# Performance work log

Measured on AMD Instinct MI355X. Metric: run time of the kernel, lower is better.

The kernel has to match this reference:

```python
import jax, jax.numpy as jnp
import numpy as np

DMODEL = 2048
NUM_HEADS = 16
NUM_KV_HEADS = 4
HEAD_DIM = DMODEL // NUM_HEADS  # 128
THETA = 10000.0


def setup_inputs() -> dict:
    key = jax.random.key(0)
    k0, k1, k2, k3, k4 = jax.random.split(key, 5)
    B, S = 1, 4096
    x = jax.random.normal(k0, (B, S, DMODEL), dtype=jnp.float32)
    # Linear weights stored as [in, out] (equivalent to torch [out,in] with x @ W.T)
    sd = 0.02
    wq = jax.random.normal(k1, (DMODEL, NUM_HEADS * HEAD_DIM), dtype=jnp.float32) * sd
    wk = jax.random.normal(k2, (DMODEL, NUM_KV_HEADS * HEAD_DIM), dtype=jnp.float32) * sd
    wv = jax.random.normal(k3, (DMODEL, NUM_KV_HEADS * HEAD_DIM), dtype=jnp.float32) * sd
    wo = jax.random.normal(k4, (NUM_HEADS * HEAD_DIM, DMODEL), dtype=jnp.float32) * sd
    return {"x": x, "wq": wq, "wk": wk, "wv": wv, "wo": wo}


def _rope_cos_sin(seqlen, dtype):
    # RoPE.forward: inv_freq over half the head dim, emb = cat(freqs, freqs)
    inv_freq = 1.0 / (THETA ** (jnp.arange(0, HEAD_DIM, 2, dtype=jnp.float32) / HEAD_DIM))
    pos = jnp.arange(seqlen, dtype=jnp.float32)
    freqs = pos[:, None] * inv_freq[None, :]          # [S, HEAD_DIM/2]
    emb = jnp.concatenate([freqs, freqs], axis=-1)    # [S, HEAD_DIM]
    return emb.astype(dtype) * 0 + jnp.cos(emb).astype(dtype), jnp.sin(emb).astype(dtype)


def _rot(t):
    half = t.shape[-1] // 2
    return jnp.concatenate([-t[..., half:], t[..., :half]], axis=-1)


def reference(x, wq, wk, wv, wo):
    B, S, _ = x.shape
    q = (x @ wq).reshape(B, S, NUM_HEADS, HEAD_DIM).transpose(0, 2, 1, 3)      # [B,H,S,D]
    k = (x @ wk).reshape(B, S, NUM_KV_HEADS, HEAD_DIM).transpose(0, 2, 1, 3)   # [B,KV,S,D]
    v = (x @ wv).reshape(B, S, NUM_KV_HEADS, HEAD_DIM).transpose(0, 2, 1, 3)

    cos, sin = _rope_cos_sin(S, x.dtype)  # [S, D]
    cos = cos[None, None, :, :]
    sin = sin[None, None, :, :]
    q = q * cos + _rot(q) * sin
    k = k * cos + _rot(k) * sin

    rep = NUM_HEADS // NUM_KV_HEADS
    k = jnp.repeat(k, rep, axis=1)  # [B,H,S,D]
    v = jnp.repeat(v, rep, axis=1)

    scale = 1.0 / jnp.sqrt(jnp.asarray(HEAD_DIM, dtype=x.dtype))
    scores = jnp.einsum('bhqd,bhkd->bhqk', q, k) * scale
    causal = jnp.tril(jnp.ones((S, S), dtype=bool))
    scores = jnp.where(causal[None, None], scores, jnp.finfo(x.dtype).min)
    attn = jax.nn.softmax(scores, axis=-1)
    o = jnp.einsum('bhqk,bhkd->bhqd', attn, v)          # [B,H,S,D]
    o = o.transpose(0, 2, 1, 3).reshape(B, S, NUM_HEADS * HEAD_DIM)
    return o @ wo
```

## Files before the change

kernel.cpp:

```cpp
#include <hip/hip_runtime.h>
#include <math.h>

#define SEQ   4096
#define DM    2048
#define NH    16
#define NKV   4
#define HD    128
#define QKVN  3072
#define CEXP  0.12753643f

typedef _Float16 f16;
typedef _Float16 f16x8 __attribute__((ext_vector_type(8)));
typedef _Float16 f16x4v __attribute__((ext_vector_type(4)));
typedef float    f32x4 __attribute__((ext_vector_type(4)));

#define GLD16(g, l) __builtin_amdgcn_global_load_lds(                        \
    (const __attribute__((address_space(1))) unsigned int*)(g),              \
    (__attribute__((address_space(3))) unsigned int*)(l), 16, 0, 0)

__global__ __launch_bounds__(256) void cast_f32_f16_k(const float* __restrict__ in,
                                                      f16* __restrict__ out, int n4)
{
    int i = blockIdx.x * 256 + threadIdx.x;
    if (i >= n4) return;
    float4 v = ((const float4*)in)[i];
    f16x4v h = {(f16)v.x, (f16)v.y, (f16)v.z, (f16)v.w};
    ((f16x4v*)out)[i] = h;
}

__global__ __launch_bounds__(256) void transpose_cast_k(const float* __restrict__ in,
                                                        f16* __restrict__ out,
                                                        int R, int Cn, float scale)
{
    __shared__ float tile[32][33];
    int bx = blockIdx.x * 32, by = blockIdx.y * 32;
    int tx = threadIdx.x & 31, ty = threadIdx.x >> 5;
    #pragma unroll
    for (int i = 0; i < 32; i += 8)
        tile[ty + i][tx] = in[(size_t)(by + ty + i) * Cn + bx + tx];
    __syncthreads();
    #pragma unroll
    for (int i = 0; i < 32; i += 8)
        out[(size_t)(bx + ty + i) * R + by + tx] = (f16)(tile[tx][ty + i] * scale);
}

__global__ __launch_bounds__(256) void transpose_f16_k(const f16* __restrict__ in,
                                                       f16* __restrict__ out,
                                                       int R, int Cn, int ldin)
{
    __shared__ f16 tile[32][33];
    int bx = blockIdx.x * 32, by = blockIdx.y * 32;
    int tx = threadIdx.x & 31, ty = threadIdx.x >> 5;
    #pragma unroll
    for (int i = 0; i < 32; i += 8)
        tile[ty + i][tx] = in[(size_t)(by + ty + i) * ldin + bx + tx];
    __syncthreads();
    #pragma unroll
    for (int i = 0; i < 32; i += 8)
        out[(size_t)(bx + ty + i) * R + by + tx] = tile[tx][ty + i];
}

template <int BN, typename OutT>
__global__ __launch_bounds__(512, 2) void gemm8p(const f16* __restrict__ A,
                                                 const f16* __restrict__ Bt,
                                                 OutT* __restrict__ C,
                                                 int M, int N, int K)
{
    constexpr int LB  = (BN == 256) ? 2 : 1;
    constexpr int NF  = BN / 16;
    constexpr int NPP = NF / 4;
    (void)M;

    __shared__ __align__(16) f16 sm[32768 + 2 * BN * 64];
    f16* As = sm;
    f16* Bs = sm + 32768;

    const int t = threadIdx.x;
    const int w = t >> 6;
    const int lane = t & 63, ln = lane & 15, quad = lane >> 4;
    const size_t bm = (size_t)blockIdx.y * 256, bn = (size_t)blockIdx.x * BN;

    auto stageA = [&](int half, int nb, size_t kn) {
        #pragma unroll
        for (int cc = 0; cc < 2; ++cc) {
            int pos = cc * 512 + t;
            int rl  = pos >> 3;
            int sc  = (pos & 7) ^ (rl & 7);
            GLD16(A + (bm + half * 128 + rl) * (size_t)K + kn + sc * 8,
                  As + nb * 16384 + half * 8192 + pos * 8);
        }
    };
    auto stageB = [&](int half, int nb, size_t kn) {
        #pragma unroll
        for (int cc = 0; cc < LB; ++cc) {
            int pos = cc * 512 + t;
            int rl  = pos >> 3;
            int sc  = (pos & 7) ^ (rl & 7);
            GLD16(Bt + (bn + half * (BN / 2) + rl) * (size_t)K + kn + sc * 8,
                  Bs + nb * (BN * 64) + half * (BN * 32) + pos * 8);
        }
    };

    f32x4 acc[2][NF];
    #pragma unroll
    for (int i = 0; i < 2; ++i)
        #pragma unroll
        for (int j = 0; j < NF; ++j) acc[i][j] = (f32x4){0.f, 0.f, 0.f, 0.f};

    const int KT = K >> 6;

    stageA(0, 0, 0); stageA(1, 0, 0); stageB(0, 0, 0); stageB(1, 0, 0);
    asm volatile("s_waitcnt vmcnt(0)" ::: "memory");
    __builtin_amdgcn_s_barrier();

    f16x8 af[2][2];

    for (int kt = 0; kt < KT; ++kt) {
        const int b = kt & 1, nb = b ^ 1;
        const size_t kn = (size_t)((kt + 1 < KT) ? (kt + 1) * 64 : (KT - 1) * 64);
        const int Ab = b * 16384, Bb = b * (BN * 64);

        #pragma unroll
        for (int q = 0; q < 4; ++q) {
            if (q == 0) {
                #pragma unroll
                for (int i = 0; i < 2; ++i)
                    #pragma unroll
                    for (int kk = 0; kk < 2; ++kk)
                        af[i][kk] = *(const f16x8*)&As[Ab + (w * 32 + i * 16 + ln) * 64
                                                         + ((kk * 4 + quad) ^ (ln & 7)) * 8];
            }
            f16x8 bf[NPP][2];
            #pragma unroll
            for (int jj = 0; jj < NPP; ++jj)
                #pragma unroll
                for (int kk = 0; kk < 2; ++kk)
                    bf[jj][kk] = *(const f16x8*)&Bs[Bb + ((q * NPP + jj) * 16 + ln) * 64
                                                       + ((kk * 4 + quad) ^ (ln & 7)) * 8];

            if (q == 0) stageA(0, nb, kn);
            if (q == 1) stageA(1, nb, kn);
            if (q == 2) stageB(0, nb, kn);
            if (q == 3) stageB(1, nb, kn);

            if (q == 1) asm volatile("s_waitcnt vmcnt(4)" ::: "memory");
            if (q == 3) {
                if constexpr (LB == 2) asm volatile("s_waitcnt vmcnt(2)" ::: "memory");
                else                   asm volatile("s_waitcnt vmcnt(1)" ::: "memory");
            }

            __builtin_amdgcn_sched_barrier(0);
            __builtin_amdgcn_s_barrier();
            __builtin_amdgcn_sched_barrier(0);
            __builtin_amdgcn_s_setprio(1);
            #pragma unroll
            for (int jj = 0; jj < NPP; ++jj)
                #pragma unroll
                for (int i = 0; i < 2; ++i)
                    #pragma unroll
                    for (int kk = 0; kk < 2; ++kk)
                        acc[i][q * NPP + jj] = __builtin_amdgcn_mfma_f32_16x16x32_f16(
                            af[i][kk], bf[jj][kk], acc[i][q * NPP + jj], 0, 0, 0);
            __builtin_amdgcn_s_setprio(0);
            __builtin_amdgcn_sched_barrier(0);
        }
    }

    #pragma unroll
    for (int i = 0; i < 2; ++i)
        #pragma unroll
        for (int j = 0; j < NF; ++j)
            #pragma unroll
            for (int r = 0; r < 4; ++r)
                C[(bm + w * 32 + i * 16 + quad * 4 + r) * (size_t)N + bn + j * 16 + ln]
                    = (OutT)acc[i][j][r];
}

__global__ __launch_bounds__(256) void rope_k(f16* __restrict__ qkv)
{
    const int s = blockIdx.x * 4 + (threadIdx.x >> 6);
    const int i = threadIdx.x & 63;
    float inv = __builtin_exp2f((float)i * -0.20762050f);
    float ang = (float)s * inv;
    float c = cosf(ang), sn = sinf(ang);
    f16* row = qkv + (size_t)s * QKVN;
    #pragma unroll
    for (int hh = 0; hh < NH + NKV; ++hh) {
        f16* base = (hh < NH) ? row + hh * HD
                              : row + DM + (hh - NH) * HD;
        float x0 = (float)base[i], x1 = (float)base[i + 64];
        base[i]      = (f16)(x0 * c - x1 * sn);
        base[i + 64] = (f16)(x1 * c + x0 * sn);
    }
}

__global__ __launch_bounds__(256, 2) void flash_k(const f16* __restrict__ qkv,
                                                  const f16* __restrict__ vt,
                                                  f16* __restrict__ O0,
                                                  f16* __restrict__ O1,
                                                  float* __restrict__ lpart)
{
    const int bid  = blockIdx.x;
    const int xcd  = bid & 7;
    const int rr   = bid >> 3;
    const int kvh  = xcd >> 1;
    const int h    = kvh * 4 + (xcd & 1) * 2 + (rr & 1);
    const int px   = (rr >> 1) & 15;
    const int half = rr >> 5;

    const int t = threadIdx.x, w = t >> 6, lane = t & 63, ln = lane & 15, quad = lane >> 4;

    f16*   Op = half ? O1 : O0;
    float* lp = lpart + (size_t)half * NH * SEQ + (size_t)h * SEQ;

    __shared__ __align__(16) f16 sm[40960];
    f16* Ps = sm + 32768 + w * 2048;

    const int glo = half * 33;
    const int ghi = glo + 33;

    int krow[4], kc[4], vrow[4], vc[4];
    #pragma unroll
    for (int cc = 0; cc < 4; ++cc) {
        int pos = cc * 256 + t;
        krow[cc] = pos >> 4; kc[cc] = (pos & 15) ^ (krow[cc] & 15);
        vrow[cc] = pos >> 3; vc[cc] = (pos & 7) ^ (vrow[cc] & 7);
    }

    #pragma unroll
    for (int ph = 0; ph < 2; ++ph) {
        const int bx   = ph ? (31 - px) : px;
        const int q0   = bx * 128;
        const int ntp  = 2 * bx + 2;
        const int base = ph ? (2 * px + 2) : 0;
        int tb_lo = glo - base; if (tb_lo < 0) tb_lo = 0;
        int tb_hi = ghi - base; if (tb_hi > ntp) tb_hi = ntp;

        const f16* kp[4]; const f16* vp[4];
        #pragma unroll
        for (int cc = 0; cc < 4; ++cc) {
            kp[cc] = qkv + (size_t)(tb_lo * 64 + krow[cc]) * QKVN + DM + kvh * HD + kc[cc] * 8;
            vp[cc] = vt  + (size_t)(kvh * HD + vrow[cc]) * SEQ + tb_lo * 64 + vc[cc] * 8;
        }
        auto stage = [&](int b) {
            f16* Kd = sm + b * 8192;
            f16* Vd = sm + 16384 + b * 8192;
            #pragma unroll
            for (int cc = 0; cc < 4; ++cc) {
                GLD16(kp[cc], Kd + (cc * 256 + t) * 8);
                GLD16(vp[cc], Vd + (cc * 256 + t) * 8);
                kp[cc] += 64 * QKVN;
                vp[cc] += 64;
            }
        };

        f16x8 qf[2][4];
        #pragma unroll
        for (int rf = 0; rf < 2; ++rf) {
            const f16* qrow = qkv + (size_t)(q0 + w * 32 + rf * 16 + ln) * QKVN + h * HD;
            #pragma unroll
            for (int tt = 0; tt < 4; ++tt)
                qf[rf][tt] = *(const f16x8*)(qrow + tt * 32 + quad * 8);
        }

        float l_r[2][4] = {{0.f, 0.f, 0.f, 0.f}, {0.f, 0.f, 0.f, 0.f}};
        f32x4 oacc[2][8];
        #pragma unroll
        for (int rf = 0; rf < 2; ++rf)
            #pragma unroll
            for (int dt = 0; dt < 8; ++dt) oacc[rf][dt] = (f32x4){0.f, 0.f, 0.f, 0.f};

        if (tb_lo < tb_hi) stage(0);
        __syncthreads();

        for (int tb = tb_lo; tb < tb_hi; ++tb) {
            const int cur = (tb - tb_lo) & 1;
            if (tb + 1 < tb_hi) stage(cur ^ 1);

            const f16* Ks  = sm + cur * 8192;
            const f16* Vts = sm + 16384 + cur * 8192;

            f32x4 sacc[2][4];
            #pragma unroll
            for (int rf = 0; rf < 2; ++rf)
                #pragma unroll
                for (int c2 = 0; c2 < 4; ++c2) sacc[rf][c2] = (f32x4){0.f, 0.f, 0.f, 0.f};
            #pragma unroll
            for (int tt = 0; tt < 4; ++tt) {
                #pragma unroll
                for (int c2 = 0; c2 < 4; ++c2) {
                    f16x8 bk = *(const f16x8*)&Ks[(c2 * 16 + ln) * 128 + ((tt * 4 + quad) ^ ln) * 8];
                    sacc[0][c2] = __builtin_amdgcn_mfma_f32_16x16x32_f16(qf[0][tt], bk, sacc[0][c2], 0, 0, 0);
                    sacc[1][c2] = __builtin_amdgcn_mfma_f32_16x16x32_f16(qf[1][tt], bk, sacc[1][c2], 0, 0, 0);
                }
            }

            if (tb >= ntp - 2) {
                const int ko = (tb - (ntp - 2)) * 64;
                #pragma unroll
                for (int rf = 0; rf < 2; ++rf)
                    #pragma unroll
                    for (int c2 = 0; c2 < 4; ++c2)
                        #pragma unroll
                        for (int r = 0; r < 4; ++r)
                            if (c2 * 16 + ln + ko > w * 32 + rf * 16 + quad * 4 + r)
                                sacc[rf][c2][r] = -INFINITY;
            }

            #pragma unroll
            for (int rf = 0; rf < 2; ++rf)
                #pragma unroll
                for (int c2 = 0; c2 < 4; ++c2)
                    #pragma unroll
                    for (int r = 0; r < 4; ++r) {
                        float e = __builtin_exp2f(sacc[rf][c2][r]);
                        l_r[rf][r] += e;
                        int row = rf * 16 + quad * 4 + r;
                        int slot = (c2 * 2 + (ln >> 3)) ^ (row & 7);
                        Ps[row * 64 + slot * 8 + (ln & 7)] = (f16)e;
                    }

            #pragma unroll
            for (int t2 = 0; t2 < 2; ++t2) {
                f16x8 pa0 = *(const f16x8*)&Ps[(0 * 16 + ln) * 64 + ((t2 * 4 + quad) ^ (ln & 7)) * 8];
                f16x8 pa1 = *(const f16x8*)&Ps[(1 * 16 + ln) * 64 + ((t2 * 4 + quad) ^ (ln & 7)) * 8];
                #pragma unroll
                for (int dt = 0; dt < 8; ++dt) {
                    f16x8 bv = *(const f16x8*)&Vts[(dt * 16 + ln) * 64 + ((t2 * 4 + quad) ^ (ln & 7)) * 8];
                    oacc[0][dt] = __builtin_amdgcn_mfma_f32_16x16x32_f16(pa0, bv, oacc[0][dt], 0, 0, 0);
                    oacc[1][dt] = __builtin_amdgcn_mfma_f32_16x16x32_f16(pa1, bv, oacc[1][dt], 0, 0, 0);
                }
            }

            __syncthreads();
        }

        #pragma unroll
        for (int rf = 0; rf < 2; ++rf)
            #pragma unroll
            for (int r = 0; r < 4; ++r) {
                float l = l_r[rf][r];
                l += __shfl_xor(l, 1, 64);
                l += __shfl_xor(l, 2, 64);
                l += __shfl_xor(l, 4, 64);
                l += __shfl_xor(l, 8, 64);
                if (ln == 0)
                    lp[q0 + w * 32 + rf * 16 + quad * 4 + r] = l;
            }
        #pragma unroll
        for (int rf = 0; rf < 2; ++rf)
            #pragma unroll
            for (int dt = 0; dt < 8; ++dt)
                #pragma unroll
                for (int r = 0; r < 4; ++r)
                    Op[(size_t)(q0 + w * 32 + rf * 16 + quad * 4 + r) * DM + h * HD + dt * 16 + ln]
                        = (f16)oacc[rf][dt][r];
    }
}

__global__ __launch_bounds__(256) void merge_k(const f16* __restrict__ O0,
                                               const f16* __restrict__ O1,
                                               const float* __restrict__ l0,
                                               const float* __restrict__ l1,
                                               f16* __restrict__ oh)
{
    int idx = blockIdx.x * 256 + threadIdx.x;
    int row = idx >> 8;
    int hh  = (idx & 255) >> 4;
    float li = 1.0f / (l0[hh * SEQ + row] + l1[hh * SEQ + row]);
    f16x8 a = ((const f16x8*)O0)[idx];
    f16x8 b = ((const f16x8*)O1)[idx];
    f16x8 o;
    #pragma unroll
    for (int i = 0; i < 8; ++i)
        o[i] = (f16)(((float)a[i] + (float)b[i]) * li);
    ((f16x8*)oh)[idx] = o;
}

extern "C" void kernel_launch(void* const* d_in, const int* in_sizes, int n_in,
                              void* d_out, int out_size, void* d_ws, size_t ws_size,
                              hipStream_t stream)
{
    (void)in_sizes; (void)n_in; (void)out_size; (void)ws_size;
    const float* x  = (const float*)d_in[0];
    const float* wq = (const float*)d_in[1];
    const float* wk = (const float*)d_in[2];
    const float* wv = (const float*)d_in[3];
    const float* wo = (const float*)d_in[4];
    float* out = (float*)d_out;

    f16* xh    = (f16*)d_ws;
    f16* wtqkv = xh + 8388608ull;
    f16* wot   = wtqkv + 6291456ull;
    f16* qkvb  = wot + 4194304ull;
    f16* vtb   = qkvb + 12582912ull;
    f16* O1    = vtb + 2097152ull;
    f16* O0    = xh;
    f16* oh    = xh;
    float* lbuf = (float*)wtqkv;

    cast_f32_f16_k<<<8192, 256, 0, stream>>>(x, xh, 2097152);
    transpose_cast_k<<<dim3(64, 64), 256, 0, stream>>>(wq, wtqkv, 2048, 2048, CEXP);
    transpose_cast_k<<<dim3(16, 64), 256, 0, stream>>>(wk, wtqkv + 2048ull * 2048, 2048, 512, 1.0f);
    transpose_cast_k<<<dim3(16, 64), 256, 0, stream>>>(wv, wtqkv + 2560ull * 2048, 2048, 512, 1.0f);
    transpose_cast_k<<<dim3(64, 64), 256, 0, stream>>>(wo, wot, 2048, 2048, 1.0f);

    gemm8p<256, f16><<<dim3(12, 16), 512, 0, stream>>>(xh, wtqkv, qkvb, 4096, 3072, 2048);
    rope_k<<<1024, 256, 0, stream>>>(qkvb);
    transpose_f16_k<<<dim3(16, 128), 256, 0, stream>>>(qkvb + 2560, vtb, 4096, 512, 3072);
    flash_k<<<dim3(512), 256, 0, stream>>>(qkvb, vtb, O0, O1, lbuf);
    merge_k<<<4096, 256, 0, stream>>>(O0, O1, lbuf, lbuf + (size_t)NH * SEQ, oh);
    gemm8p<128, float><<<dim3(16, 16), 512, 0, stream>>>(oh, wot, out, 4096, 2048, 2048);
}
```

Measured before the change: 342.8 us.

## Split flash attention KV range three ways and read V directly from global

Splits the flash-attention key range into three partial blocks instead of two when the workspace is large enough, adding a third output buffer and a three-way merge. V tiles are no longer staged through shared memory; each lane loads V fragments straight from the transposed V buffer in global memory. This shrinks LDS use and raises the occupancy target to 3 blocks per CU. The trade-off is uncached global loads of V on the inner MFMA loop and extra merge traffic.

```diff
diff --git a/kernel.cpp b/kernel.cpp
--- a/kernel.cpp
+++ b/kernel.cpp
@@ -194,11 +194,13 @@
     }
 }
 
-__global__ __launch_bounds__(256, 2) void flash_k(const f16* __restrict__ qkv,
+__global__ __launch_bounds__(256, 3) void flash_k(const f16* __restrict__ qkv,
                                                   const f16* __restrict__ vt,
                                                   f16* __restrict__ O0,
                                                   f16* __restrict__ O1,
-                                                  float* __restrict__ lpart)
+                                                  f16* __restrict__ O2,
+                                                  float* __restrict__ lpart,
+                                                  int tpb)
 {
     const int bid  = blockIdx.x;
     const int xcd  = bid & 7;
@@ -210,22 +212,23 @@
 
     const int t = threadIdx.x, w = t >> 6, lane = t & 63, ln = lane & 15, quad = lane >> 4;
 
-    f16*   Op = half ? O1 : O0;
+    f16*   Op = (half == 0) ? O0 : (half == 1) ? O1 : O2;
     float* lp = lpart + (size_t)half * NH * SEQ + (size_t)h * SEQ;
 
-    __shared__ __align__(16) f16 sm[40960];
-    f16* Ps = sm + 32768 + w * 2048;
-
-    const int glo = half * 33;
-    const int ghi = glo + 33;
-
-    int krow[4], kc[4], vrow[4], vc[4];
+    __shared__ __align__(16) f16 sm[24576];
+    f16* Ps = sm + 16384 + w * 2048;
+
+    const int glo = half * tpb;
+    const int ghi = glo + tpb;
+
+    int krow[4], kc[4];
     #pragma unroll
     for (int cc = 0; cc < 4; ++cc) {
         int pos = cc * 256 + t;
         krow[cc] = pos >> 4; kc[cc] = (pos & 15) ^ (krow[cc] & 15);
-        vrow[cc] = pos >> 3; vc[cc] = (pos & 7) ^ (vrow[cc] & 7);
     }
+
+    const f16* vbase = vt + (size_t)kvh * HD * SEQ;
 
     #pragma unroll
     for (int ph = 0; ph < 2; ++ph) {
@@ -236,21 +239,16 @@
         int tb_lo = glo - base; if (tb_lo < 0) tb_lo = 0;
         int tb_hi = ghi - base; if (tb_hi > ntp) tb_hi = ntp;
 
-        const f16* kp[4]; const f16* vp[4];
-        #pragma unroll
-        for (int cc = 0; cc < 4; ++cc) {
+        const f16* kp[4];
+        #pragma unroll
+        for (int cc = 0; cc < 4; ++cc)
             kp[cc] = qkv + (size_t)(tb_lo * 64 + krow[cc]) * QKVN + DM + kvh * HD + kc[cc] * 8;
-            vp[cc] = vt  + (size_t)(kvh * HD + vrow[cc]) * SEQ + tb_lo * 64 + vc[cc] * 8;
-        }
         auto stage = [&](int b) {
             f16* Kd = sm + b * 8192;
-            f16* Vd = sm + 16384 + b * 8192;
             #pragma unroll
             for (int cc = 0; cc < 4; ++cc) {
                 GLD16(kp[cc], Kd + (cc * 256 + t) * 8);
-                GLD16(vp[cc], Vd + (cc * 256 + t) * 8);
                 kp[cc] += 64 * QKVN;
-                vp[cc] += 64;
             }
         };
 
@@ -277,8 +275,8 @@
             const int cur = (tb - tb_lo) & 1;
             if (tb + 1 < tb_hi) stage(cur ^ 1);
 
-            const f16* Ks  = sm + cur * 8192;
-            const f16* Vts = sm + 16384 + cur * 8192;
+            const f16* Ks = sm + cur * 8192;
+            const int  kb = tb * 64;
 
             f32x4 sacc[2][4];
             #pragma unroll
@@ -326,7 +324,8 @@
                 f16x8 pa1 = *(const f16x8*)&Ps[(1 * 16 + ln) * 64 + ((t2 * 4 + quad) ^ (ln & 7)) * 8];
                 #pragma unroll
                 for (int dt = 0; dt < 8; ++dt) {
-                    f16x8 bv = *(const f16x8*)&Vts[(dt * 16 + ln) * 64 + ((t2 * 4 + quad) ^ (ln & 7)) * 8];
+                    f16x8 bv = *(const f16x8*)(vbase + (size_t)(dt * 16 + ln) * SEQ
+                                               + kb + t2 * 32 + quad * 8);
                     oacc[0][dt] = __builtin_amdgcn_mfma_f32_16x16x32_f16(pa0, bv, oacc[0][dt], 0, 0, 0);
                     oacc[1][dt] = __builtin_amdgcn_mfma_f32_16x16x32_f16(pa1, bv, oacc[1][dt], 0, 0, 0);
                 }
@@ -358,22 +357,35 @@
     }
 }
 
+template <int S>
 __global__ __launch_bounds__(256) void merge_k(const f16* __restrict__ O0,
                                                const f16* __restrict__ O1,
-                                               const float* __restrict__ l0,
-                                               const float* __restrict__ l1,
+                                               const f16* __restrict__ O2,
+                                               const float* __restrict__ lbuf,
                                                f16* __restrict__ oh)
 {
     int idx = blockIdx.x * 256 + threadIdx.x;
     int row = idx >> 8;
     int hh  = (idx & 255) >> 4;
-    float li = 1.0f / (l0[hh * SEQ + row] + l1[hh * SEQ + row]);
+    float s = 0.f;
+    #pragma unroll
+    for (int si = 0; si < S; ++si)
+        s += lbuf[(size_t)si * NH * SEQ + hh * SEQ + row];
+    float li = 1.0f / s;
     f16x8 a = ((const f16x8*)O0)[idx];
     f16x8 b = ((const f16x8*)O1)[idx];
     f16x8 o;
-    #pragma unroll
-    for (int i = 0; i < 8; ++i)
-        o[i] = (f16)(((float)a[i] + (float)b[i]) * li);
+    if constexpr (S == 3) {
+        f16x8 c = ((const f16x8*)O2)[idx];
+        #pragma unroll
+        for (int i = 0; i < 8; ++i)
+            o[i] = (f16)(((float)a[i] + (float)b[i] + (float)c[i]) * li);
+    } else {
+        (void)O2;
+        #pragma unroll
+        for (int i = 0; i < 8; ++i)
+            o[i] = (f16)(((float)a[i] + (float)b[i]) * li);
+    }
     ((f16x8*)oh)[idx] = o;
 }
 
@@ -381,7 +393,7 @@
                               void* d_out, int out_size, void* d_ws, size_t ws_size,
                               hipStream_t stream)
 {
-    (void)in_sizes; (void)n_in; (void)out_size; (void)ws_size;
+    (void)in_sizes; (void)n_in; (void)out_size;
     const float* x  = (const float*)d_in[0];
     const float* wq = (const float*)d_in[1];
     const float* wk = (const float*)d_in[2];
@@ -399,6 +411,11 @@
     f16* oh    = xh;
     float* lbuf = (float*)wtqkv;
 
+    const bool big = ws_size >= 100663296ull;
+    f16* O2 = big ? (O1 + 8388608ull) : O1;
+    const int nsplit = big ? 3 : 2;
+    const int tpb    = 66 / nsplit;
+
     cast_f32_f16_k<<<8192, 256, 0, stream>>>(x, xh, 2097152);
     transpose_cast_k<<<dim3(64, 64), 256, 0, stream>>>(wq, wtqkv, 2048, 2048, CEXP);
     transpose_cast_k<<<dim3(16, 64), 256, 0, stream>>>(wk, wtqkv + 2048ull * 2048, 2048, 512, 1.0f);
@@ -408,7 +425,8 @@
     gemm8p<256, f16><<<dim3(12, 16), 512, 0, stream>>>(xh, wtqkv, qkvb, 4096, 3072, 2048);
     rope_k<<<1024, 256, 0, stream>>>(qkvb);
     transpose_f16_k<<<dim3(16, 128), 256, 0, stream>>>(qkvb + 2560, vtb, 4096, 512, 3072);
-    flash_k<<<dim3(512), 256, 0, stream>>>(qkvb, vtb, O0, O1, lbuf);
-    merge_k<<<4096, 256, 0, stream>>>(O0, O1, lbuf, lbuf + (size_t)NH * SEQ, oh);
+    flash_k<<<dim3(256 * nsplit), 256, 0, stream>>>(qkvb, vtb, O0, O1, O2, lbuf, tpb);
+    if (big) merge_k<3><<<4096, 256, 0, stream>>>(O0, O1, O2, lbuf, oh);
+    else     merge_k<2><<<4096, 256, 0, stream>>>(O0, O1, O1, lbuf, oh);
     gemm8p<128, float><<<dim3(16, 16), 512, 0, stream>>>(oh, wot, out, 4096, 2048, 2048);
 }
```

Result: slower. 616.7 us (+79.9%).
